# Performance work log

Measured on AMD Instinct MI355X. Metric: run time of the kernel, lower is better.

The kernel has to match this reference:

```python
import jax, jax.numpy as jnp
import numpy as np

B, K, H, L = 50000, 32, 128, 64
KL_BETA = 0.001
LN_EPS = 1e-5


def _layernorm(x, g, b):
    m = jnp.mean(x, axis=-1, keepdims=True)
    v = jnp.mean((x - m) ** 2, axis=-1, keepdims=True)
    return (x - m) * jax.lax.rsqrt(v + LN_EPS) * g + b


def setup_inputs() -> dict:
    key = jax.random.key(0)
    ks = jax.random.split(key, 16)
    s = 0.05
    return {
        "self_feat": jax.random.normal(ks[0], (B, H), jnp.float32),
        "neighbor_feat": jax.random.normal(ks[1], (B, K, H), jnp.float32),
        "trust_mask": jax.random.uniform(ks[2], (B, K, 1), jnp.float32),
        "eps": jax.random.normal(ks[3], (B, K, L), jnp.float32),
        "pre_g": jnp.ones((H,), jnp.float32), "pre_b": jnp.zeros((H,), jnp.float32),
        "W_mu": jax.random.normal(ks[4], (H, L), jnp.float32) * s, "b_mu": jnp.zeros((L,), jnp.float32),
        "W_lv": jax.random.normal(ks[5], (H, L), jnp.float32) * s, "b_lv": jnp.zeros((L,), jnp.float32),
        "post_g": jnp.ones((L,), jnp.float32), "post_b": jnp.zeros((L,), jnp.float32),
        "W_q": jax.random.normal(ks[6], (H, L), jnp.float32) * s, "b_q": jnp.zeros((L,), jnp.float32),
        "W_k": jax.random.normal(ks[7], (L, L), jnp.float32) * s, "b_k": jnp.zeros((L,), jnp.float32),
        "W_v": jax.random.normal(ks[8], (L, L), jnp.float32) * s, "b_v": jnp.zeros((L,), jnp.float32),
        "W_o": jax.random.normal(ks[9], (L, H), jnp.float32) * s, "b_o": jnp.zeros((H,), jnp.float32),
    }


def reference(self_feat, neighbor_feat, trust_mask, eps,
              pre_g, pre_b, W_mu, b_mu, W_lv, b_lv, post_g, post_b,
              W_q, b_q, W_k, b_k, W_v, b_v, W_o, b_o):
    # [B,K,H] -> layernorm -> VIB reparameterization -> [B,K,L]
    nn = _layernorm(neighbor_feat, pre_g, pre_b)
    mu = nn @ W_mu + b_mu                      # [B,K,L]
    logvar = nn @ W_lv + b_lv                  # [B,K,L]
    z = mu + eps * jnp.exp(0.5 * logvar)       # reparam
    z = _layernorm(z, post_g, post_b)
    # trust-masked single-query attention over K neighbors
    q = self_feat @ W_q + b_q                  # [B,L]
    k = z @ W_k + b_k                          # [B,K,L]
    v = z @ W_v + b_v                          # [B,K,L]
    logits = jnp.einsum("bl,bkl->bk", q, k) / jnp.sqrt(jnp.float32(L))
    logits = logits + jnp.log(trust_mask[..., 0] + 1e-6)
    attn = jax.nn.softmax(logits, axis=-1)     # [B,K]
    context = jnp.einsum("bk,bkl->bl", attn, v)
    comm_feat = context @ W_o + b_o            # [B,H]
    kl = -0.5 * jnp.mean(jnp.sum(1.0 + logvar - mu ** 2 - jnp.exp(logvar), axis=-1))
    return comm_feat, KL_BETA * kl
```

## Files before the change

### kernel.cpp

```cpp
#include <hip/hip_runtime.h>
#include <hip/hip_bf16.h>

typedef float f32x4 __attribute__((ext_vector_type(4)));
typedef short bf16x8 __attribute__((ext_vector_type(8)));

#define NB 50000
#define NK 32
#define NH 128
#define NL 64

static __device__ __forceinline__ unsigned short f2bf(float f) {
    unsigned int u = __float_as_uint(f);
    u += 0x7fffu + ((u >> 16) & 1u);
    return (unsigned short)(u >> 16);
}
static __device__ __forceinline__ float bf2f(unsigned short u) {
    return __uint_as_float(((unsigned int)u) << 16);
}
static __device__ __forceinline__ float bflo(unsigned int u) { return __uint_as_float(u << 16); }
static __device__ __forceinline__ float bfhi(unsigned int u) { return __uint_as_float(u & 0xffff0000u); }

__global__ void kl_zero_kernel(float* out) {
    if (threadIdx.x == 0 && blockIdx.x == 0) out[(size_t)NB * NH] = 0.0f;
}

__global__ void __launch_bounds__(256) q_kernel(const float* __restrict__ self_feat,
                                                const float* __restrict__ W_q,
                                                const float* __restrict__ b_q,
                                                unsigned short* __restrict__ q_ws)
{
    __shared__ __align__(16) unsigned short A[32 * 128];
    const int t = threadIdx.x, w = t >> 6, l = t & 63, g = l >> 4, li = l & 15;

    bf16x8 Bq[4];
#pragma unroll
    for (int s = 0; s < 4; ++s) {
        int k0 = 32 * s + 8 * g, c = li + 16 * w;
        bf16x8 f;
#pragma unroll
        for (int j = 0; j < 8; ++j) f[j] = (short)f2bf(W_q[(k0 + j) * 64 + c]);
        Bq[s] = f;
    }
    const float bq = b_q[li + 16 * w];
    const int n0 = blockIdx.x * 32;

    {
        int row = t >> 3, c0 = (t & 7) * 16;
        float x[16];
        if (n0 + row < NB) {
            const float* src = self_feat + (size_t)(n0 + row) * NH + c0;
#pragma unroll
            for (int i = 0; i < 4; ++i) {
                float4 v4 = ((const float4*)src)[i];
                x[4 * i] = v4.x; x[4 * i + 1] = v4.y; x[4 * i + 2] = v4.z; x[4 * i + 3] = v4.w;
            }
        } else {
#pragma unroll
            for (int i = 0; i < 16; ++i) x[i] = 0.f;
        }
        alignas(16) unsigned short yb[16];
#pragma unroll
        for (int i = 0; i < 16; ++i) yb[i] = f2bf(x[i]);
        int boff = row * 256 + c0 * 2;
        *(int4*)((char*)A + ((boff) ^ ((row & 7) << 4))) = *(int4*)&yb[0];
        *(int4*)((char*)A + ((boff + 16) ^ ((row & 7) << 4))) = *(int4*)&yb[8];
    }
    __syncthreads();

    const f32x4 zero4 = {0.f, 0.f, 0.f, 0.f};
    f32x4 acc[2] = {zero4, zero4};
#pragma unroll
    for (int s = 0; s < 4; ++s) {
        bf16x8 A0 = *(const bf16x8*)((const char*)A + ((li * 256 + s * 64 + g * 16) ^ ((li & 7) << 4)));
        bf16x8 A1 = *(const bf16x8*)((const char*)A + (((16 + li) * 256 + s * 64 + g * 16) ^ ((li & 7) << 4)));
        acc[0] = __builtin_amdgcn_mfma_f32_16x16x32_bf16(A0, Bq[s], acc[0], 0, 0, 0);
        acc[1] = __builtin_amdgcn_mfma_f32_16x16x32_bf16(A1, Bq[s], acc[1], 0, 0, 0);
    }
#pragma unroll
    for (int mt = 0; mt < 2; ++mt)
#pragma unroll
        for (int r = 0; r < 4; ++r) {
            int row = 16 * mt + 4 * g + r;
            if (n0 + row < NB)
                q_ws[(size_t)(n0 + row) * 64 + li + 16 * w] = f2bf(acc[mt][r] + bq);
        }
}

__global__ void __launch_bounds__(256) ka_kernel(
    const float* __restrict__ neighbor_feat, const float* __restrict__ eps_g,
    const float* __restrict__ pre_g, const float* __restrict__ pre_b,
    const float* __restrict__ W_mu, const float* __restrict__ b_mu,
    const float* __restrict__ W_lv, const float* __restrict__ b_lv,
    const float* __restrict__ post_g, const float* __restrict__ post_b,
    unsigned short* __restrict__ z_ws, float* __restrict__ out,
    int nbeg, int ncnt)
{
    __shared__ __align__(16) unsigned short A[32 * 128];
    __shared__ float muv[32 * 136];
    __shared__ float2 s_pgb[128];
    __shared__ float s_bmu[64], s_blv[64], s_pg[64], s_pb[64];
    __shared__ float klw[4];

    const int t = threadIdx.x, w = t >> 6, l = t & 63, g = l >> 4, li = l & 15;

    if (t < 128) s_pgb[t] = make_float2(pre_g[t], pre_b[t]);
    if (t < 64) { s_bmu[t] = b_mu[t]; s_blv[t] = b_lv[t]; s_pg[t] = post_g[t]; s_pb[t] = post_b[t]; }

    bf16x8 Wml[2][4];
    {
        const float* Wsrc = (w < 2) ? W_mu : W_lv;
        int cb = 32 * (w & 1) + li;
#pragma unroll
        for (int ntp = 0; ntp < 2; ++ntp)
#pragma unroll
            for (int s = 0; s < 4; ++s) {
                int k0 = 32 * s + 8 * g, c = cb + 16 * ntp;
                bf16x8 f;
#pragma unroll
                for (int j = 0; j < 8; ++j) f[j] = (short)f2bf(Wsrc[(k0 + j) * 64 + c]);
                Wml[ntp][s] = f;
            }
    }
    __syncthreads();

    const int row = t >> 3;
    const int c0 = (t & 7) * 16;
    const int l0 = (t & 7) * 8;
    const int nend = nbeg + ncnt;
    int bn = nbeg + blockIdx.x * 8;

    float x[16], ee[8];
    {
        int bs = (bn < nend) ? bn : nbeg;
        const float* src = neighbor_feat + ((size_t)bs * NK + row) * NH + c0;
#pragma unroll
        for (int i = 0; i < 4; ++i) {
            float4 v4 = ((const float4*)src)[i];
            x[4 * i] = v4.x; x[4 * i + 1] = v4.y; x[4 * i + 2] = v4.z; x[4 * i + 3] = v4.w;
        }
        const float* ep = eps_g + ((size_t)bs * NK + row) * NL + l0;
        float4 e0 = ((const float4*)ep)[0], e1 = ((const float4*)ep)[1];
        ee[0] = e0.x; ee[1] = e0.y; ee[2] = e0.z; ee[3] = e0.w;
        ee[4] = e1.x; ee[5] = e1.y; ee[6] = e1.z; ee[7] = e1.w;
    }

    float kl_acc = 0.f;
    const f32x4 zero4 = {0.f, 0.f, 0.f, 0.f};

    for (int i = 0; i < 8; ++i, ++bn) {
        const bool live = (bn < nend);
        const int bnx = (bn + 1 < nend) ? bn + 1 : nbeg;

        float s1 = 0.f;
#pragma unroll
        for (int j = 0; j < 16; ++j) s1 += x[j];
        s1 += __shfl_xor(s1, 1); s1 += __shfl_xor(s1, 2); s1 += __shfl_xor(s1, 4);
        float mean = s1 * (1.f / 128.f);
        float s2 = 0.f;
#pragma unroll
        for (int j = 0; j < 16; ++j) { float d = x[j] - mean; s2 += d * d; }
        s2 += __shfl_xor(s2, 1); s2 += __shfl_xor(s2, 2); s2 += __shfl_xor(s2, 4);
        float inv = rsqrtf(s2 * (1.f / 128.f) + 1e-5f);
        alignas(16) unsigned short yb[16];
#pragma unroll
        for (int j = 0; j < 16; ++j) {
            float2 gb = s_pgb[c0 + j];
            yb[j] = f2bf((x[j] - mean) * inv * gb.x + gb.y);
        }
        {
            int boff = row * 256 + c0 * 2;
            *(int4*)((char*)A + ((boff) ^ ((row & 7) << 4))) = *(int4*)&yb[0];
            *(int4*)((char*)A + ((boff + 16) ^ ((row & 7) << 4))) = *(int4*)&yb[8];
        }
        {
            const float* src = neighbor_feat + ((size_t)bnx * NK + row) * NH + c0;
#pragma unroll
            for (int j = 0; j < 4; ++j) {
                float4 v4 = ((const float4*)src)[j];
                x[4 * j] = v4.x; x[4 * j + 1] = v4.y; x[4 * j + 2] = v4.z; x[4 * j + 3] = v4.w;
            }
        }
        __syncthreads();

        f32x4 acc[2][2];
        acc[0][0] = zero4; acc[0][1] = zero4; acc[1][0] = zero4; acc[1][1] = zero4;
#pragma unroll
        for (int s = 0; s < 4; ++s) {
            bf16x8 A0 = *(const bf16x8*)((const char*)A + ((li * 256 + s * 64 + g * 16) ^ ((li & 7) << 4)));
            bf16x8 A1 = *(const bf16x8*)((const char*)A + (((16 + li) * 256 + s * 64 + g * 16) ^ ((li & 7) << 4)));
#pragma unroll
            for (int ntp = 0; ntp < 2; ++ntp) {
                acc[0][ntp] = __builtin_amdgcn_mfma_f32_16x16x32_bf16(A0, Wml[ntp][s], acc[0][ntp], 0, 0, 0);
                acc[1][ntp] = __builtin_amdgcn_mfma_f32_16x16x32_bf16(A1, Wml[ntp][s], acc[1][ntp], 0, 0, 0);
            }
        }
#pragma unroll
        for (int mt = 0; mt < 2; ++mt)
#pragma unroll
            for (int ntp = 0; ntp < 2; ++ntp)
#pragma unroll
                for (int r = 0; r < 4; ++r)
                    muv[(16 * mt + 4 * g + r) * 136 + 32 * w + 16 * ntp + li] = acc[mt][ntp][r];
        __syncthreads();

        f32x4 mu0 = *(const f32x4*)&muv[row * 136 + l0];
        f32x4 mu1 = *(const f32x4*)&muv[row * 136 + l0 + 4];
        f32x4 lv0 = *(const f32x4*)&muv[row * 136 + 64 + l0];
        f32x4 lv1 = *(const f32x4*)&muv[row * 136 + 64 + l0 + 4];
        float zr[8];
#pragma unroll
        for (int j = 0; j < 8; ++j) {
            float mu = ((j < 4) ? mu0[j & 3] : mu1[j & 3]) + s_bmu[l0 + j];
            float lv = ((j < 4) ? lv0[j & 3] : lv1[j & 3]) + s_blv[l0 + j];
            float eh = __expf(0.5f * lv);
            if (live) kl_acc += 1.f + lv - mu * mu - eh * eh;
            zr[j] = mu + ee[j] * eh;
        }
        {
            const float* ep = eps_g + ((size_t)bnx * NK + row) * NL + l0;
            float4 e0 = ((const float4*)ep)[0], e1 = ((const float4*)ep)[1];
            ee[0] = e0.x; ee[1] = e0.y; ee[2] = e0.z; ee[3] = e0.w;
            ee[4] = e1.x; ee[5] = e1.y; ee[6] = e1.z; ee[7] = e1.w;
        }
        float zs = 0.f;
#pragma unroll
        for (int j = 0; j < 8; ++j) zs += zr[j];
        zs += __shfl_xor(zs, 1); zs += __shfl_xor(zs, 2); zs += __shfl_xor(zs, 4);
        float zm = zs * (1.f / 64.f);
        float zv = 0.f;
#pragma unroll
        for (int j = 0; j < 8; ++j) { float d = zr[j] - zm; zv += d * d; }
        zv += __shfl_xor(zv, 1); zv += __shfl_xor(zv, 2); zv += __shfl_xor(zv, 4);
        float zi = rsqrtf(zv * (1.f / 64.f) + 1e-5f);
        alignas(16) unsigned short zb[8];
#pragma unroll
        for (int j = 0; j < 8; ++j)
            zb[j] = f2bf((zr[j] - zm) * zi * s_pg[l0 + j] + s_pb[l0 + j]);
        if (live)
            *(int4*)(z_ws + (size_t)(bn - nbeg) * (NK * NL) + row * NL + l0) = *(int4*)zb;
    }

#pragma unroll
    for (int msk = 1; msk < 64; msk <<= 1) kl_acc += __shfl_xor(kl_acc, msk);
    if (l == 0) klw[w] = kl_acc;
    __syncthreads();
    if (t == 0) {
        float tot = klw[0] + klw[1] + klw[2] + klw[3];
        atomicAdd(out + (size_t)NB * NH, tot * (-0.5f * 0.001f / ((float)NB * NK)));
    }
}

__global__ void __launch_bounds__(256) kb_kernel(
    const unsigned short* __restrict__ z_ws, const float* __restrict__ trust_mask,
    const unsigned short* __restrict__ q_ws,
    const float* __restrict__ W_k, const float* __restrict__ W_v,
    const float* __restrict__ b_v,
    const float* __restrict__ W_o, const float* __restrict__ b_o,
    float* __restrict__ out, int nbeg, int ncnt)
{
    __shared__ uint4 WkvB[8 * 2 * 64];
    __shared__ uint2 WoP[32 * 64];
    __shared__ float ctxl[4][64];

    const int t = threadIdx.x, w = t >> 6, l = t & 63, g = l >> 4, li = l & 15;

    for (int e = t; e < 1024; e += 256) {
        int nt = e >> 7, s = (e >> 6) & 1, ln = e & 63;
        const float* src = (nt < 4) ? W_k : W_v;
        int gg = ln >> 4, ll = ln & 15, c = ll + 16 * (nt & 3);
        unsigned int p[4];
#pragma unroll
        for (int jp = 0; jp < 4; ++jp) {
            int k = 32 * s + 8 * gg + 2 * jp;
            p[jp] = (unsigned)f2bf(src[k * 64 + c]) | ((unsigned)f2bf(src[(k + 1) * 64 + c]) << 16);
        }
        WkvB[e] = make_uint4(p[0], p[1], p[2], p[3]);
    }
    for (int e = t; e < 2048; e += 256) {
        int c2 = e >> 6, h = e & 63;
        unsigned int w0 = (unsigned)f2bf(W_o[(2 * c2) * 128 + h]) | ((unsigned)f2bf(W_o[(2 * c2) * 128 + h + 64]) << 16);
        unsigned int w1 = (unsigned)f2bf(W_o[(2 * c2 + 1) * 128 + h]) | ((unsigned)f2bf(W_o[(2 * c2 + 1) * 128 + h + 64]) << 16);
        WoP[e] = make_uint2(w0, w1);
    }
    float bv4[4];
#pragma unroll
    for (int nt = 0; nt < 4; ++nt) bv4[nt] = b_v[li + 16 * nt];
    const float bo0 = b_o[l], bo1 = b_o[64 + l];
    __syncthreads();

    const int nend = nbeg + ncnt;
    const int stride = gridDim.x * 4;
    int bn = nbeg + blockIdx.x * 4 + w;

    bf16x8 za0[2], za1[2];
    float q4[4], trr;
    {
        int bs = (bn < nend) ? bn : nbeg;
        const unsigned short* zp = z_ws + (size_t)(bs - nbeg) * (NK * NL);
#pragma unroll
        for (int s = 0; s < 2; ++s) {
            za0[s] = *(const bf16x8*)(zp + li * NL + 32 * s + 8 * g);
            za1[s] = *(const bf16x8*)(zp + (16 + li) * NL + 32 * s + 8 * g);
        }
#pragma unroll
        for (int nt = 0; nt < 4; ++nt) q4[nt] = bf2f(q_ws[(size_t)bs * 64 + li + 16 * nt]);
        trr = trust_mask[(size_t)bs * NK + (l & 31)];
    }

    const f32x4 zero4 = {0.f, 0.f, 0.f, 0.f};

    for (; bn < nend; bn += stride) {
        const int nx = (bn + stride < nend) ? bn + stride : bn;

        f32x4 acck[2][4];
#pragma unroll
        for (int mt = 0; mt < 2; ++mt)
#pragma unroll
            for (int nt = 0; nt < 4; ++nt) acck[mt][nt] = zero4;
#pragma unroll
        for (int s = 0; s < 2; ++s)
#pragma unroll
            for (int nt = 0; nt < 4; ++nt) {
                bf16x8 fb = *(const bf16x8*)&WkvB[(nt * 2 + s) * 64 + l];
                acck[0][nt] = __builtin_amdgcn_mfma_f32_16x16x32_bf16(za0[s], fb, acck[0][nt], 0, 0, 0);
                acck[1][nt] = __builtin_amdgcn_mfma_f32_16x16x32_bf16(za1[s], fb, acck[1][nt], 0, 0, 0);
            }
        float trlog = __logf(trr + 1e-6f);
        float att[2][4];
#pragma unroll
        for (int mt = 0; mt < 2; ++mt)
#pragma unroll
            for (int r = 0; r < 4; ++r) {
                float p = q4[0] * acck[mt][0][r] + q4[1] * acck[mt][1][r]
                        + q4[2] * acck[mt][2][r] + q4[3] * acck[mt][3][r];
                p += __shfl_xor(p, 1); p += __shfl_xor(p, 2);
                p += __shfl_xor(p, 4); p += __shfl_xor(p, 8);
                att[mt][r] = p * 0.125f + __shfl(trlog, 16 * mt + 4 * g + r);
            }
        float m = att[0][0];
#pragma unroll
        for (int mt = 0; mt < 2; ++mt)
#pragma unroll
            for (int r = 0; r < 4; ++r) m = fmaxf(m, att[mt][r]);
        m = fmaxf(m, __shfl_xor(m, 16)); m = fmaxf(m, __shfl_xor(m, 32));
        float den = 0.f;
#pragma unroll
        for (int mt = 0; mt < 2; ++mt)
#pragma unroll
            for (int r = 0; r < 4; ++r) { att[mt][r] = __expf(att[mt][r] - m); den += att[mt][r]; }
        den += __shfl_xor(den, 16); den += __shfl_xor(den, 32);
        float idn = 1.f / den;

        f32x4 accv[2][4];
#pragma unroll
        for (int mt = 0; mt < 2; ++mt)
#pragma unroll
            for (int nt = 0; nt < 4; ++nt) accv[mt][nt] = zero4;
#pragma unroll
        for (int s = 0; s < 2; ++s)
#pragma unroll
            for (int nt = 0; nt < 4; ++nt) {
                bf16x8 fb = *(const bf16x8*)&WkvB[((nt + 4) * 2 + s) * 64 + l];
                accv[0][nt] = __builtin_amdgcn_mfma_f32_16x16x32_bf16(za0[s], fb, accv[0][nt], 0, 0, 0);
                accv[1][nt] = __builtin_amdgcn_mfma_f32_16x16x32_bf16(za1[s], fb, accv[1][nt], 0, 0, 0);
            }
        {
            const unsigned short* zp = z_ws + (size_t)(nx - nbeg) * (NK * NL);
#pragma unroll
            for (int s = 0; s < 2; ++s) {
                za0[s] = *(const bf16x8*)(zp + li * NL + 32 * s + 8 * g);
                za1[s] = *(const bf16x8*)(zp + (16 + li) * NL + 32 * s + 8 * g);
            }
#pragma unroll
            for (int nt = 0; nt < 4; ++nt) q4[nt] = bf2f(q_ws[(size_t)nx * 64 + li + 16 * nt]);
            trr = trust_mask[(size_t)nx * NK + (l & 31)];
        }

#pragma unroll
        for (int nt = 0; nt < 4; ++nt) {
            float cx = 0.f;
#pragma unroll
            for (int mt = 0; mt < 2; ++mt)
#pragma unroll
                for (int r = 0; r < 4; ++r) cx += att[mt][r] * idn * accv[mt][nt][r];
            cx += __shfl_xor(cx, 16); cx += __shfl_xor(cx, 32);
            if (g == 0) ctxl[w][li + 16 * nt] = cx + bv4[nt];
        }

        float o0 = 0.f, o1 = 0.f;
#pragma unroll
        for (int c2 = 0; c2 < 32; ++c2) {
            float2 cc = *(const float2*)&ctxl[w][2 * c2];
            uint2 W2 = WoP[c2 * 64 + l];
            o0 += cc.x * bflo(W2.x) + cc.y * bflo(W2.y);
            o1 += cc.x * bfhi(W2.x) + cc.y * bfhi(W2.y);
        }
        out[(size_t)bn * NH + l] = o0 + bo0;
        out[(size_t)bn * NH + 64 + l] = o1 + bo1;
    }
}

extern "C" void kernel_launch(void* const* d_in, const int* in_sizes, int n_in,
                              void* d_out, int out_size, void* d_ws, size_t ws_size,
                              hipStream_t stream) {
    const float* self_feat     = (const float*)d_in[0];
    const float* neighbor_feat = (const float*)d_in[1];
    const float* trust_mask    = (const float*)d_in[2];
    const float* eps           = (const float*)d_in[3];
    const float* pre_g  = (const float*)d_in[4];
    const float* pre_b  = (const float*)d_in[5];
    const float* W_mu   = (const float*)d_in[6];
    const float* b_mu   = (const float*)d_in[7];
    const float* W_lv   = (const float*)d_in[8];
    const float* b_lv   = (const float*)d_in[9];
    const float* post_g = (const float*)d_in[10];
    const float* post_b = (const float*)d_in[11];
    const float* W_q    = (const float*)d_in[12];
    const float* b_q    = (const float*)d_in[13];
    const float* W_k    = (const float*)d_in[14];
    const float* W_v    = (const float*)d_in[16];
    const float* b_v    = (const float*)d_in[17];
    const float* W_o    = (const float*)d_in[18];
    const float* b_o    = (const float*)d_in[19];
    float* out = (float*)d_out;

    unsigned short* q_ws = (unsigned short*)d_ws;
    const size_t qbytes = (size_t)NB * NL * sizeof(unsigned short);
    unsigned short* z_ws = (unsigned short*)((char*)d_ws + qbytes);
    size_t zcap = (ws_size > qbytes) ? (ws_size - qbytes) : 0;
    long long chunk = (long long)(zcap / ((size_t)NK * NL * sizeof(unsigned short)));
    chunk &= ~7LL;
    if (chunk > NB) chunk = NB;
    if (chunk < 8) chunk = 8;

    hipLaunchKernelGGL(kl_zero_kernel, dim3(1), dim3(64), 0, stream, out);
    hipLaunchKernelGGL(q_kernel, dim3((NB + 31) / 32), dim3(256), 0, stream, self_feat, W_q, b_q, q_ws);

    for (int beg = 0; beg < NB; beg += (int)chunk) {
        int cnt = (NB - beg < (int)chunk) ? (NB - beg) : (int)chunk;
        hipLaunchKernelGGL(ka_kernel, dim3((cnt + 7) / 8), dim3(256), 0, stream,
                           neighbor_feat, eps, pre_g, pre_b,
                           W_mu, b_mu, W_lv, b_lv, post_g, post_b,
                           z_ws, out, beg, cnt);
        int gb = (cnt + 3) / 4; if (gb > 768) gb = 768;
        hipLaunchKernelGGL(kb_kernel, dim3(gb), dim3(256), 0, stream,
                           z_ws, trust_mask, q_ws,
                           W_k, W_v, b_v, W_o, b_o, out, beg, cnt);
    }
}
```

Before: 433.0 us.

## Fold W_k into query and W_v·W_o into one matrix, fuse attention into z kernel

Precomputes q·W_kᵀ per batch row and the combined W_v·W_o matrix with its bias, so logits become a dot product of z with a precomputed vector. The context is a weighted average of z passed through a single 64x128 projection. This lets the z-producing kernel finish attention and the output projection in place. That removes the bf16 z workspace round trip, the chunked loop and the separate kb kernel. The b_k term is dropped, which is exact because it adds a constant to every logit and cancels in softmax. The cost is more shared-memory syncs per batch row and a single-block kernel that builds the fused weights.

```diff
diff --git a/kernel.cpp b/kernel.cpp
--- a/kernel.cpp
+++ b/kernel.cpp
@@ -24,12 +24,37 @@
     if (threadIdx.x == 0 && blockIdx.x == 0) out[(size_t)NB * NH] = 0.0f;
 }
 
-__global__ void __launch_bounds__(256) q_kernel(const float* __restrict__ self_feat,
-                                                const float* __restrict__ W_q,
-                                                const float* __restrict__ b_q,
-                                                unsigned short* __restrict__ q_ws)
+__global__ void __launch_bounds__(256) wvo_kernel(const float* __restrict__ W_v,
+                                                  const float* __restrict__ W_o,
+                                                  const float* __restrict__ b_v,
+                                                  const float* __restrict__ b_o,
+                                                  float* __restrict__ wvo_ws,
+                                                  float* __restrict__ bvo_ws)
+{
+    const int t = threadIdx.x;
+    for (int e = t; e < 64 * 128; e += 256) {
+        int d = e >> 7, h = e & 127;
+        float s = 0.f;
+#pragma unroll 8
+        for (int c = 0; c < 64; ++c) s += W_v[d * 64 + c] * W_o[c * 128 + h];
+        wvo_ws[e] = s;
+    }
+    if (t < 128) {
+        float s = b_o[t];
+#pragma unroll 8
+        for (int c = 0; c < 64; ++c) s += b_v[c] * W_o[c * 128 + t];
+        bvo_ws[t] = s;
+    }
+}
+
+__global__ void __launch_bounds__(256) qk_kernel(const float* __restrict__ self_feat,
+                                                 const float* __restrict__ W_q,
+                                                 const float* __restrict__ b_q,
+                                                 const float* __restrict__ W_k,
+                                                 float* __restrict__ qk_ws)
 {
     __shared__ __align__(16) unsigned short A[32 * 128];
+    __shared__ __align__(16) unsigned short ZQ[32 * 64];
     const int t = threadIdx.x, w = t >> 6, l = t & 63, g = l >> 4, li = l & 15;
 
     bf16x8 Bq[4];
@@ -40,6 +65,15 @@
 #pragma unroll
         for (int j = 0; j < 8; ++j) f[j] = (short)f2bf(W_q[(k0 + j) * 64 + c]);
         Bq[s] = f;
+    }
+    bf16x8 Bk[2];
+#pragma unroll
+    for (int s = 0; s < 2; ++s) {
+        int k0 = 32 * s + 8 * g, d = li + 16 * w;
+        bf16x8 f;
+#pragma unroll
+        for (int j = 0; j < 8; ++j) f[j] = (short)f2bf(W_k[d * 64 + k0 + j]);
+        Bk[s] = f;
     }
     const float bq = b_q[li + 16 * w];
     const int n0 = blockIdx.x * 32;
@@ -80,32 +114,59 @@
     for (int mt = 0; mt < 2; ++mt)
 #pragma unroll
         for (int r = 0; r < 4; ++r) {
+            int row = 16 * mt + 4 * g + r, c = li + 16 * w;
+            *(unsigned short*)((char*)ZQ + ((row * 128 + c * 2) ^ ((row & 7) << 4))) = f2bf(acc[mt][r] + bq);
+        }
+    __syncthreads();
+
+    f32x4 acc2[2] = {zero4, zero4};
+#pragma unroll
+    for (int s = 0; s < 2; ++s) {
+        bf16x8 A0 = *(const bf16x8*)((const char*)ZQ + ((li * 128 + s * 64 + g * 16) ^ ((li & 7) << 4)));
+        bf16x8 A1 = *(const bf16x8*)((const char*)ZQ + (((16 + li) * 128 + s * 64 + g * 16) ^ (((16 + li) & 7) << 4)));
+        acc2[0] = __builtin_amdgcn_mfma_f32_16x16x32_bf16(A0, Bk[s], acc2[0], 0, 0, 0);
+        acc2[1] = __builtin_amdgcn_mfma_f32_16x16x32_bf16(A1, Bk[s], acc2[1], 0, 0, 0);
+    }
+#pragma unroll
+    for (int mt = 0; mt < 2; ++mt)
+#pragma unroll
+        for (int r = 0; r < 4; ++r) {
             int row = 16 * mt + 4 * g + r;
             if (n0 + row < NB)
-                q_ws[(size_t)(n0 + row) * 64 + li + 16 * w] = f2bf(acc[mt][r] + bq);
-        }
-}
-
-__global__ void __launch_bounds__(256) ka_kernel(
-    const float* __restrict__ neighbor_feat, const float* __restrict__ eps_g,
+                qk_ws[(size_t)(n0 + row) * 64 + li + 16 * w] = acc2[mt][r];
+        }
+}
+
+__global__ void __launch_bounds__(256) fz_kernel(
+    const float* __restrict__ neighbor_feat, const float* __restrict__ trust_mask,
+    const float* __restrict__ eps_g,
     const float* __restrict__ pre_g, const float* __restrict__ pre_b,
     const float* __restrict__ W_mu, const float* __restrict__ b_mu,
     const float* __restrict__ W_lv, const float* __restrict__ b_lv,
     const float* __restrict__ post_g, const float* __restrict__ post_b,
-    unsigned short* __restrict__ z_ws, float* __restrict__ out,
-    int nbeg, int ncnt)
+    const float* __restrict__ qk_ws, const float* __restrict__ wvo_ws,
+    const float* __restrict__ bvo_ws,
+    float* __restrict__ out)
 {
     __shared__ __align__(16) unsigned short A[32 * 128];
     __shared__ float muv[32 * 136];
+    __shared__ unsigned int WvoP[64 * 64];
     __shared__ float2 s_pgb[128];
     __shared__ float s_bmu[64], s_blv[64], s_pg[64], s_pb[64];
+    __shared__ float bvo_l[128];
+    __shared__ float logit_l[32];
+    __shared__ float zpart[4][64];
+    __shared__ float zbar_l[64];
     __shared__ float klw[4];
 
     const int t = threadIdx.x, w = t >> 6, l = t & 63, g = l >> 4, li = l & 15;
 
-    if (t < 128) s_pgb[t] = make_float2(pre_g[t], pre_b[t]);
+    if (t < 128) { s_pgb[t] = make_float2(pre_g[t], pre_b[t]); bvo_l[t] = bvo_ws[t]; }
     if (t < 64) { s_bmu[t] = b_mu[t]; s_blv[t] = b_lv[t]; s_pg[t] = post_g[t]; s_pb[t] = post_b[t]; }
-
+    for (int e = t; e < 4096; e += 256) {
+        int c = e >> 6, hp = e & 63;
+        WvoP[e] = (unsigned)f2bf(wvo_ws[c * 128 + hp]) | ((unsigned)f2bf(wvo_ws[c * 128 + hp + 64]) << 16);
+    }
     bf16x8 Wml[2][4];
     {
         const float* Wsrc = (w < 2) ? W_mu : W_lv;
@@ -126,30 +187,32 @@
     const int row = t >> 3;
     const int c0 = (t & 7) * 16;
     const int l0 = (t & 7) * 8;
-    const int nend = nbeg + ncnt;
-    int bn = nbeg + blockIdx.x * 8;
-
-    float x[16], ee[8];
+    int bn = blockIdx.x * 8;
+
+    float x[16], ee[8], qk8[8], trr;
     {
-        int bs = (bn < nend) ? bn : nbeg;
-        const float* src = neighbor_feat + ((size_t)bs * NK + row) * NH + c0;
+        const float* src = neighbor_feat + ((size_t)bn * NK + row) * NH + c0;
 #pragma unroll
         for (int i = 0; i < 4; ++i) {
             float4 v4 = ((const float4*)src)[i];
             x[4 * i] = v4.x; x[4 * i + 1] = v4.y; x[4 * i + 2] = v4.z; x[4 * i + 3] = v4.w;
         }
-        const float* ep = eps_g + ((size_t)bs * NK + row) * NL + l0;
+        const float* ep = eps_g + ((size_t)bn * NK + row) * NL + l0;
         float4 e0 = ((const float4*)ep)[0], e1 = ((const float4*)ep)[1];
         ee[0] = e0.x; ee[1] = e0.y; ee[2] = e0.z; ee[3] = e0.w;
         ee[4] = e1.x; ee[5] = e1.y; ee[6] = e1.z; ee[7] = e1.w;
+        const float* qp = qk_ws + (size_t)bn * 64 + l0;
+        float4 q0 = ((const float4*)qp)[0], q1 = ((const float4*)qp)[1];
+        qk8[0] = q0.x; qk8[1] = q0.y; qk8[2] = q0.z; qk8[3] = q0.w;
+        qk8[4] = q1.x; qk8[5] = q1.y; qk8[6] = q1.z; qk8[7] = q1.w;
+        trr = trust_mask[(size_t)bn * NK + row];
     }
 
     float kl_acc = 0.f;
     const f32x4 zero4 = {0.f, 0.f, 0.f, 0.f};
 
     for (int i = 0; i < 8; ++i, ++bn) {
-        const bool live = (bn < nend);
-        const int bnx = (bn + 1 < nend) ? bn + 1 : nbeg;
+        const int bnx = (bn + 1 < NB) ? bn + 1 : bn;
 
         float s1 = 0.f;
 #pragma unroll
@@ -213,7 +276,7 @@
             float mu = ((j < 4) ? mu0[j & 3] : mu1[j & 3]) + s_bmu[l0 + j];
             float lv = ((j < 4) ? lv0[j & 3] : lv1[j & 3]) + s_blv[l0 + j];
             float eh = __expf(0.5f * lv);
-            if (live) kl_acc += 1.f + lv - mu * mu - eh * eh;
+            kl_acc += 1.f + lv - mu * mu - eh * eh;
             zr[j] = mu + ee[j] * eh;
         }
         {
@@ -232,12 +295,62 @@
         for (int j = 0; j < 8; ++j) { float d = zr[j] - zm; zv += d * d; }
         zv += __shfl_xor(zv, 1); zv += __shfl_xor(zv, 2); zv += __shfl_xor(zv, 4);
         float zi = rsqrtf(zv * (1.f / 64.f) + 1e-5f);
-        alignas(16) unsigned short zb[8];
 #pragma unroll
         for (int j = 0; j < 8; ++j)
-            zb[j] = f2bf((zr[j] - zm) * zi * s_pg[l0 + j] + s_pb[l0 + j]);
-        if (live)
-            *(int4*)(z_ws + (size_t)(bn - nbeg) * (NK * NL) + row * NL + l0) = *(int4*)zb;
+            zr[j] = (zr[j] - zm) * zi * s_pg[l0 + j] + s_pb[l0 + j];
+
+        float lg = 0.f;
+#pragma unroll
+        for (int j = 0; j < 8; ++j) lg += zr[j] * qk8[j];
+        lg += __shfl_xor(lg, 1); lg += __shfl_xor(lg, 2); lg += __shfl_xor(lg, 4);
+        if ((l & 7) == 0) logit_l[row] = lg * 0.125f + __logf(trr + 1e-6f);
+        {
+            const float* qp = qk_ws + (size_t)bnx * 64 + l0;
+            float4 q0 = ((const float4*)qp)[0], q1 = ((const float4*)qp)[1];
+            qk8[0] = q0.x; qk8[1] = q0.y; qk8[2] = q0.z; qk8[3] = q0.w;
+            qk8[4] = q1.x; qk8[5] = q1.y; qk8[6] = q1.z; qk8[7] = q1.w;
+            trr = trust_mask[(size_t)bnx * NK + row];
+        }
+        __syncthreads();
+
+        float mx = logit_l[0];
+#pragma unroll
+        for (int n = 1; n < 32; ++n) mx = fmaxf(mx, logit_l[n]);
+        float den = 0.f;
+#pragma unroll
+        for (int n = 0; n < 32; ++n) den += __expf(logit_l[n] - mx);
+        float att = __expf(logit_l[row] - mx) / den;
+
+        float av[8];
+#pragma unroll
+        for (int j = 0; j < 8; ++j) av[j] = att * zr[j];
+#pragma unroll
+        for (int j = 0; j < 8; ++j) {
+            av[j] += __shfl_xor(av[j], 8);
+            av[j] += __shfl_xor(av[j], 16);
+            av[j] += __shfl_xor(av[j], 32);
+        }
+        if (l < 8) {
+            float4 p0 = {av[0], av[1], av[2], av[3]};
+            float4 p1 = {av[4], av[5], av[6], av[7]};
+            ((float4*)&zpart[w][8 * l])[0] = p0;
+            ((float4*)&zpart[w][8 * l])[1] = p1;
+        }
+        __syncthreads();
+
+        if (t < 64) zbar_l[t] = zpart[0][t] + zpart[1][t] + zpart[2][t] + zpart[3][t];
+        __syncthreads();
+
+        if (t < 128) {
+            int hp = t & 63, hi = t >> 6;
+            float o = 0.f;
+#pragma unroll 8
+            for (int c = 0; c < 64; ++c) {
+                unsigned int W2 = WvoP[c * 64 + hp];
+                o += zbar_l[c] * (hi ? bfhi(W2) : bflo(W2));
+            }
+            out[(size_t)bn * NH + 64 * hi + hp] = o + bvo_l[64 * hi + hp];
+        }
     }
 
 #pragma unroll
@@ -247,156 +360,6 @@
     if (t == 0) {
         float tot = klw[0] + klw[1] + klw[2] + klw[3];
         atomicAdd(out + (size_t)NB * NH, tot * (-0.5f * 0.001f / ((float)NB * NK)));
-    }
-}
-
-__global__ void __launch_bounds__(256) kb_kernel(
-    const unsigned short* __restrict__ z_ws, const float* __restrict__ trust_mask,
-    const unsigned short* __restrict__ q_ws,
-    const float* __restrict__ W_k, const float* __restrict__ W_v,
-    const float* __restrict__ b_v,
-    const float* __restrict__ W_o, const float* __restrict__ b_o,
-    float* __restrict__ out, int nbeg, int ncnt)
-{
-    __shared__ uint4 WkvB[8 * 2 * 64];
-    __shared__ uint2 WoP[32 * 64];
-    __shared__ float ctxl[4][64];
-
-    const int t = threadIdx.x, w = t >> 6, l = t & 63, g = l >> 4, li = l & 15;
-
-    for (int e = t; e < 1024; e += 256) {
-        int nt = e >> 7, s = (e >> 6) & 1, ln = e & 63;
-        const float* src = (nt < 4) ? W_k : W_v;
-        int gg = ln >> 4, ll = ln & 15, c = ll + 16 * (nt & 3);
-        unsigned int p[4];
-#pragma unroll
-        for (int jp = 0; jp < 4; ++jp) {
-            int k = 32 * s + 8 * gg + 2 * jp;
-            p[jp] = (unsigned)f2bf(src[k * 64 + c]) | ((unsigned)f2bf(src[(k + 1) * 64 + c]) << 16);
-        }
-        WkvB[e] = make_uint4(p[0], p[1], p[2], p[3]);
-    }
-    for (int e = t; e < 2048; e += 256) {
-        int c2 = e >> 6, h = e & 63;
-        unsigned int w0 = (unsigned)f2bf(W_o[(2 * c2) * 128 + h]) | ((unsigned)f2bf(W_o[(2 * c2) * 128 + h + 64]) << 16);
-        unsigned int w1 = (unsigned)f2bf(W_o[(2 * c2 + 1) * 128 + h]) | ((unsigned)f2bf(W_o[(2 * c2 + 1) * 128 + h + 64]) << 16);
-        WoP[e] = make_uint2(w0, w1);
-    }
-    float bv4[4];
-#pragma unroll
-    for (int nt = 0; nt < 4; ++nt) bv4[nt] = b_v[li + 16 * nt];
-    const float bo0 = b_o[l], bo1 = b_o[64 + l];
-    __syncthreads();
-
-    const int nend = nbeg + ncnt;
-    const int stride = gridDim.x * 4;
-    int bn = nbeg + blockIdx.x * 4 + w;
-
-    bf16x8 za0[2], za1[2];
-    float q4[4], trr;
-    {
-        int bs = (bn < nend) ? bn : nbeg;
-        const unsigned short* zp = z_ws + (size_t)(bs - nbeg) * (NK * NL);
-#pragma unroll
-        for (int s = 0; s < 2; ++s) {
-            za0[s] = *(const bf16x8*)(zp + li * NL + 32 * s + 8 * g);
-            za1[s] = *(const bf16x8*)(zp + (16 + li) * NL + 32 * s + 8 * g);
-        }
-#pragma unroll
-        for (int nt = 0; nt < 4; ++nt) q4[nt] = bf2f(q_ws[(size_t)bs * 64 + li + 16 * nt]);
-        trr = trust_mask[(size_t)bs * NK + (l & 31)];
-    }
-
-    const f32x4 zero4 = {0.f, 0.f, 0.f, 0.f};
-
-    for (; bn < nend; bn += stride) {
-        const int nx = (bn + stride < nend) ? bn + stride : bn;
-
-        f32x4 acck[2][4];
-#pragma unroll
-        for (int mt = 0; mt < 2; ++mt)
-#pragma unroll
-            for (int nt = 0; nt < 4; ++nt) acck[mt][nt] = zero4;
-#pragma unroll
-        for (int s = 0; s < 2; ++s)
-#pragma unroll
-            for (int nt = 0; nt < 4; ++nt) {
-                bf16x8 fb = *(const bf16x8*)&WkvB[(nt * 2 + s) * 64 + l];
-                acck[0][nt] = __builtin_amdgcn_mfma_f32_16x16x32_bf16(za0[s], fb, acck[0][nt], 0, 0, 0);
-                acck[1][nt] = __builtin_amdgcn_mfma_f32_16x16x32_bf16(za1[s], fb, acck[1][nt], 0, 0, 0);
-            }
-        float trlog = __logf(trr + 1e-6f);
-        float att[2][4];
-#pragma unroll
-        for (int mt = 0; mt < 2; ++mt)
-#pragma unroll
-            for (int r = 0; r < 4; ++r) {
-                float p = q4[0] * acck[mt][0][r] + q4[1] * acck[mt][1][r]
-                        + q4[2] * acck[mt][2][r] + q4[3] * acck[mt][3][r];
-                p += __shfl_xor(p, 1); p += __shfl_xor(p, 2);
-                p += __shfl_xor(p, 4); p += __shfl_xor(p, 8);
-                att[mt][r] = p * 0.125f + __shfl(trlog, 16 * mt + 4 * g + r);
-            }
-        float m = att[0][0];
-#pragma unroll
-        for (int mt = 0; mt < 2; ++mt)
-#pragma unroll
-            for (int r = 0; r < 4; ++r) m = fmaxf(m, att[mt][r]);
-        m = fmaxf(m, __shfl_xor(m, 16)); m = fmaxf(m, __shfl_xor(m, 32));
-        float den = 0.f;
-#pragma unroll
-        for (int mt = 0; mt < 2; ++mt)
-#pragma unroll
-            for (int r = 0; r < 4; ++r) { att[mt][r] = __expf(att[mt][r] - m); den += att[mt][r]; }
-        den += __shfl_xor(den, 16); den += __shfl_xor(den, 32);
-        float idn = 1.f / den;
-
-        f32x4 accv[2][4];
-#pragma unroll
-        for (int mt = 0; mt < 2; ++mt)
-#pragma unroll
-            for (int nt = 0; nt < 4; ++nt) accv[mt][nt] = zero4;
-#pragma unroll
-        for (int s = 0; s < 2; ++s)
-#pragma unroll
-            for (int nt = 0; nt < 4; ++nt) {
-                bf16x8 fb = *(const bf16x8*)&WkvB[((nt + 4) * 2 + s) * 64 + l];
-                accv[0][nt] = __builtin_amdgcn_mfma_f32_16x16x32_bf16(za0[s], fb, accv[0][nt], 0, 0, 0);
-                accv[1][nt] = __builtin_amdgcn_mfma_f32_16x16x32_bf16(za1[s], fb, accv[1][nt], 0, 0, 0);
-            }
-        {
-            const unsigned short* zp = z_ws + (size_t)(nx - nbeg) * (NK * NL);
-#pragma unroll
-            for (int s = 0; s < 2; ++s) {
-                za0[s] = *(const bf16x8*)(zp + li * NL + 32 * s + 8 * g);
-                za1[s] = *(const bf16x8*)(zp + (16 + li) * NL + 32 * s + 8 * g);
-            }
-#pragma unroll
-            for (int nt = 0; nt < 4; ++nt) q4[nt] = bf2f(q_ws[(size_t)nx * 64 + li + 16 * nt]);
-            trr = trust_mask[(size_t)nx * NK + (l & 31)];
-        }
-
-#pragma unroll
-        for (int nt = 0; nt < 4; ++nt) {
-            float cx = 0.f;
-#pragma unroll
-            for (int mt = 0; mt < 2; ++mt)
-#pragma unroll
-                for (int r = 0; r < 4; ++r) cx += att[mt][r] * idn * accv[mt][nt][r];
-            cx += __shfl_xor(cx, 16); cx += __shfl_xor(cx, 32);
-            if (g == 0) ctxl[w][li + 16 * nt] = cx + bv4[nt];
-        }
-
-        float o0 = 0.f, o1 = 0.f;
-#pragma unroll
-        for (int c2 = 0; c2 < 32; ++c2) {
-            float2 cc = *(const float2*)&ctxl[w][2 * c2];
-            uint2 W2 = WoP[c2 * 64 + l];
-            o0 += cc.x * bflo(W2.x) + cc.y * bflo(W2.y);
-            o1 += cc.x * bfhi(W2.x) + cc.y * bfhi(W2.y);
-        }
-        out[(size_t)bn * NH + l] = o0 + bo0;
-        out[(size_t)bn * NH + 64 + l] = o1 + bo1;
     }
 }
 
@@ -424,27 +387,16 @@
     const float* b_o    = (const float*)d_in[19];
     float* out = (float*)d_out;
 
-    unsigned short* q_ws = (unsigned short*)d_ws;
-    const size_t qbytes = (size_t)NB * NL * sizeof(unsigned short);
-    unsigned short* z_ws = (unsigned short*)((char*)d_ws + qbytes);
-    size_t zcap = (ws_size > qbytes) ? (ws_size - qbytes) : 0;
-    long long chunk = (long long)(zcap / ((size_t)NK * NL * sizeof(unsigned short)));
-    chunk &= ~7LL;
-    if (chunk > NB) chunk = NB;
-    if (chunk < 8) chunk = 8;
+    float* qk_ws  = (float*)d_ws;
+    float* wvo_ws = qk_ws + (size_t)NB * 64;
+    float* bvo_ws = wvo_ws + 64 * 128;
 
     hipLaunchKernelGGL(kl_zero_kernel, dim3(1), dim3(64), 0, stream, out);
-    hipLaunchKernelGGL(q_kernel, dim3((NB + 31) / 32), dim3(256), 0, stream, self_feat, W_q, b_q, q_ws);
-
-    for (int beg = 0; beg < NB; beg += (int)chunk) {
-        int cnt = (NB - beg < (int)chunk) ? (NB - beg) : (int)chunk;
-        hipLaunchKernelGGL(ka_kernel, dim3((cnt + 7) / 8), dim3(256), 0, stream,
-                           neighbor_feat, eps, pre_g, pre_b,
-                           W_mu, b_mu, W_lv, b_lv, post_g, post_b,
-                           z_ws, out, beg, cnt);
-        int gb = (cnt + 3) / 4; if (gb > 768) gb = 768;
-        hipLaunchKernelGGL(kb_kernel, dim3(gb), dim3(256), 0, stream,
-                           z_ws, trust_mask, q_ws,
-                           W_k, W_v, b_v, W_o, b_o, out, beg, cnt);
-    }
-}
+    hipLaunchKernelGGL(wvo_kernel, dim3(1), dim3(256), 0, stream, W_v, W_o, b_v, b_o, wvo_ws, bvo_ws);
+    hipLaunchKernelGGL(qk_kernel, dim3((NB + 31) / 32), dim3(256), 0, stream,
+                       self_feat, W_q, b_q, W_k, qk_ws);
+    hipLaunchKernelGGL(fz_kernel, dim3(NB / 8), dim3(256), 0, stream,
+                       neighbor_feat, trust_mask, eps, pre_g, pre_b,
+                       W_mu, b_mu, W_lv, b_lv, post_g, post_b,
+                       qk_ws, wvo_ws, bvo_ws, out);
+}
```

New measurement: 613.3 us. 41.6% more time.
